# Performance work log

Measured on AMD Instinct MI355X. Metric: run time of the kernel, lower is better.

Reference implementation:

```python
import jax, jax.numpy as jnp
import numpy as np

NUM_CLASSES = 21
THRESH = 0.5
NEG_POS = 3
VAR0, VAR1 = 0.1, 0.2


def point_form(boxes):
    # center form (cx,cy,w,h) -> corner form (x1,y1,x2,y2)
    return jnp.concatenate([boxes[:, :2] - boxes[:, 2:] / 2,
                            boxes[:, :2] + boxes[:, 2:] / 2], axis=1)


def jaccard(a, b):
    # a: [N,4] corner form, b: [P,4] corner form -> IoU [N,P]
    lt = jnp.maximum(a[:, None, :2], b[None, :, :2])
    rb = jnp.minimum(a[:, None, 2:], b[None, :, 2:])
    wh = jnp.clip(rb - lt, 0.0)
    inter = wh[..., 0] * wh[..., 1]
    area_a = (a[:, 2] - a[:, 0]) * (a[:, 3] - a[:, 1])
    area_b = (b[:, 2] - b[:, 0]) * (b[:, 3] - b[:, 1])
    return inter / (area_a[:, None] + area_b[None, :] - inter)


def match_one(truths, labels, priors):
    # truths: [N,4] corner form, labels: [N] int, priors: [P,4] center form
    ov = jaccard(truths, point_form(priors))            # [N,P]
    best_prior_idx = jnp.argmax(ov, axis=1)             # [N] best prior per truth
    best_truth_ov = jnp.max(ov, axis=0)                 # [P]
    best_truth_idx = jnp.argmax(ov, axis=0)             # [P]
    # ensure each truth keeps its best prior
    best_truth_ov = best_truth_ov.at[best_prior_idx].set(2.0)
    best_truth_idx = best_truth_idx.at[best_prior_idx].set(
        jnp.arange(truths.shape[0], dtype=best_truth_idx.dtype))
    matches = truths[best_truth_idx]                    # [P,4]
    conf = labels[best_truth_idx] + 1                   # [P]
    conf = jnp.where(best_truth_ov < THRESH, 0, conf)
    # encode
    g_cxcy = ((matches[:, :2] + matches[:, 2:]) / 2 - priors[:, :2]) / (VAR0 * priors[:, 2:])
    g_wh = jnp.log((matches[:, 2:] - matches[:, :2]) / priors[:, 2:]) / VAR1
    return jnp.concatenate([g_cxcy, g_wh], axis=1), conf


def setup_inputs() -> dict:
    key = jax.random.key(0)
    k1, k2, k3, k4, k5, k6, k7 = jax.random.split(key, 7)
    B, P, C, N = 64, 24564, NUM_CLASSES, 16
    loc_data = jax.random.normal(k1, (B, P, 4), dtype=jnp.float32)
    conf_data = jax.random.normal(k2, (B, P, C), dtype=jnp.float32)
    # priors: valid center-form boxes
    ctr = 0.05 + 0.9 * jax.random.uniform(k3, (P, 2), dtype=jnp.float32)
    pwh = 0.05 + 0.25 * jax.random.uniform(k4, (P, 2), dtype=jnp.float32)
    priors = jnp.concatenate([ctr, pwh], axis=1)
    # truths: valid corner-form boxes
    xy1 = 0.7 * jax.random.uniform(k5, (B, N, 2), dtype=jnp.float32)
    twh = 0.05 + 0.2 * jax.random.uniform(k6, (B, N, 2), dtype=jnp.float32)
    truths = jnp.concatenate([xy1, xy1 + twh], axis=2)
    labels = jax.random.randint(k7, (B, N), 0, 20, dtype=jnp.int32)
    return {"loc_data": loc_data, "conf_data": conf_data, "priors": priors,
            "truths": truths, "labels": labels}


def reference(loc_data, conf_data, priors, truths, labels):
    B, P, C = conf_data.shape
    loc_t, conf_t = jax.vmap(lambda t, l: match_one(t, l, priors))(truths, labels)
    pos = conf_t > 0                                     # [B,P]

    # localization smooth-L1, summed over positives
    diff = loc_data - loc_t
    ad = jnp.abs(diff)
    sl1 = jnp.where(ad < 1.0, 0.5 * diff * diff, ad - 0.5)
    loss_l = jnp.sum(sl1 * pos[..., None].astype(loc_data.dtype))

    # per-prior CE = logsumexp - logit at matched class
    lse = jax.nn.logsumexp(conf_data, axis=2)            # [B,P]
    gathered = jnp.take_along_axis(conf_data, conf_t[..., None].astype(jnp.int32), axis=2)[..., 0]
    loss_c_all = lse - gathered

    # hard-negative mining via double argsort rank (pos zeroed first)
    loss_c_mine = jnp.where(pos, 0.0, loss_c_all)
    idx_rank = jnp.argsort(jnp.argsort(-loss_c_mine, axis=1), axis=1)
    num_pos = jnp.sum(pos, axis=1, keepdims=True)        # [B,1]
    num_neg = jnp.minimum(NEG_POS * num_pos, P - 1)
    neg = idx_rank < num_neg

    mask = pos | neg
    loss_c = jnp.sum(jnp.where(mask, loss_c_all, 0.0))

    n = jnp.sum(num_pos).astype(loc_data.dtype)
    return loss_l / n, loss_c / n
```

## Files before the change

kernel.cpp:

```cpp
#include <hip/hip_runtime.h>
#include <cstdint>
#include <cstddef>

#define B_ 64
#define P_ 24564
#define C_ 21
#define N_ 16
#define NPL_ 96
#define THRESH_ 0.5f


__device__ inline void async_copy16(const float* g, float* l) {
    __builtin_amdgcn_global_load_lds(
        (const __attribute__((address_space(1))) void*)g,
        (__attribute__((address_space(3))) void*)l, 16, 0, 0);
}

__device__ inline float sl1_encode(float4 ld, float4 pr,
                                   float tx1, float ty1, float tx2, float ty2) {
    float gcx = ((tx1 + tx2) * 0.5f - pr.x) / (0.1f * pr.z);
    float gcy = ((ty1 + ty2) * 0.5f - pr.y) / (0.1f * pr.w);
    float gw  = __logf((tx2 - tx1) / pr.z) / 0.2f;
    float gh  = __logf((ty2 - ty1) / pr.w) / 0.2f;
    float g[4] = {gcx, gcy, gw, gh};
    float l[4] = {ld.x, ld.y, ld.z, ld.w};
    float s = 0.0f;
#pragma unroll
    for (int i = 0; i < 4; i++) {
        float d = l[i] - g[i];
        float ad = fabsf(d);
        s += (ad < 1.0f) ? 0.5f * d * d : ad - 0.5f;
    }
    return s;
}


__global__ __launch_bounds__(256, 6) void
kF_fused(const float* __restrict__ loc,
         const float* __restrict__ conf,
         const float* __restrict__ priors,
         const float* __restrict__ truths,
         const int* __restrict__ labels,
         float* __restrict__ mine,
         float* __restrict__ part_ll,
         float* __restrict__ part_pce,
         int* __restrict__ part_np,
         unsigned long long* __restrict__ part_key) {
    int b = blockIdx.y, bx = blockIdx.x, t = threadIdx.x;
    int wid = t >> 6, lane = t & 63;
    __shared__ float scf[256 * C_];
    __shared__ unsigned long long swk[N_ * 4];
    __shared__ int lb[N_];
    __shared__ float sll[4], spc[4];
    __shared__ int snp[4];

    int base_p = bx * 256;
    int nvalid = min(256, P_ - base_p);
    int maxf4 = (nvalid * C_) >> 2;
    const float* gtile = conf + ((size_t)b * P_ + base_p) * C_;

    for (int k = wid; k < 21; k += 4) {
        int f4 = k * 64 + lane;
        int s4 = (f4 < maxf4) ? f4 : (maxf4 - 1);
        async_copy16(gtile + (size_t)s4 * 4, scf + k * 256);
    }
    if (t < N_) lb[t] = labels[b * N_ + t];

    int p0 = base_p + t;
    bool valid = t < nvalid;
    float4 pr = ((const float4*)priors)[valid ? p0 : base_p];
    float px1 = pr.x - pr.z * 0.5f, py1 = pr.y - pr.w * 0.5f;
    float px2 = pr.x + pr.z * 0.5f, py2 = pr.y + pr.w * 0.5f;
    float ap = (px2 - px1) * (py2 - py1);

    float best = -1.0f;
    int bn = 0;
#pragma unroll
    for (int n = 0; n < N_; n++) {
        float4 tb = ((const float4*)truths)[b * N_ + n];
        float at = (tb.z - tb.x) * (tb.w - tb.y);
        float lx = fmaxf(tb.x, px1), ly = fmaxf(tb.y, py1);
        float rx = fminf(tb.z, px2), ry = fminf(tb.w, py2);
        float w = fmaxf(rx - lx, 0.0f), h = fmaxf(ry - ly, 0.0f);
        float inter = w * h;
        float iou = inter / (at + ap - inter);
        if (iou > best) { best = iou; bn = n; }

        unsigned k32 = valid ? __float_as_uint(iou) : 0u;
        unsigned m = k32;
#pragma unroll
        for (int off = 32; off; off >>= 1) {
            unsigned o = __shfl_xor(m, off);
            m = (o > m) ? o : m;
        }
        unsigned long long msk = __ballot(k32 == m);
        int wl = (int)__ffsll(msk) - 1;
        if (lane == 0)
            swk[n * 4 + wid] = ((unsigned long long)m << 32) |
                               (unsigned)~(unsigned)(base_p + (wid << 6) + wl);
    }
    int pos = (valid && best >= THRESH_) ? 1 : 0;

    __syncthreads();

    if (t < N_) {
        unsigned long long bk = swk[t * 4];
#pragma unroll
        for (int i = 1; i < 4; i++) {
            unsigned long long o = swk[t * 4 + i];
            bk = (o > bk) ? o : bk;
        }
        part_key[(size_t)(b * NPL_ + bx) * N_ + t] = bk;
    }

    float ll = 0.0f, pce = 0.0f;
    int np = 0;
    if (valid) {
        int cls = pos ? (lb[bn] + 1) : 0;
        float ssum = 0.0f;
#pragma unroll
        for (int i = 0; i < 21; i++) ssum += __expf(scf[t * 21 + i]);
        float g = scf[t * 21 + cls];
        float lca = fmaxf(__logf(ssum) - g, 0.0f);

        mine[(size_t)b * P_ + p0] = pos ? 0.0f : lca;

        if (pos) {
            np = 1;
            pce = lca;
            float4 ld = ((const float4*)loc)[(size_t)b * P_ + p0];
            float4 tb = ((const float4*)truths)[b * N_ + bn];
            ll = sl1_encode(ld, pr, tb.x, tb.y, tb.z, tb.w);
        }
    }

    for (int off = 32; off; off >>= 1) {
        ll += __shfl_down(ll, off);
        pce += __shfl_down(pce, off);
        np += __shfl_down(np, off);
    }
    if (lane == 0) { sll[wid] = ll; spc[wid] = pce; snp[wid] = np; }
    __syncthreads();
    if (t == 0) {
        float a = 0.0f, cc = 0.0f;
        int q = 0;
        for (int i = 0; i < 4; i++) { a += sll[i]; cc += spc[i]; q += snp[i]; }
        part_ll[b * NPL_ + bx] = a;
        part_pce[b * NPL_ + bx] = cc;
        part_np[b * NPL_ + bx] = q;
    }
}

__global__ __launch_bounds__(1024) void
kB_batch(const float* __restrict__ loc,
         const float* __restrict__ conf,
         const float* __restrict__ priors,
         const float* __restrict__ truths,
         const int* __restrict__ labels,
         const float* __restrict__ mine,
         const float* __restrict__ part_ll,
         const float* __restrict__ part_pce,
         const int* __restrict__ part_np,
         const unsigned long long* __restrict__ part_key,
         double* __restrict__ bll,
         double* __restrict__ bpc,
         int* __restrict__ bnp) {
    int b = blockIdx.x, t = threadIdx.x, wid = t >> 6, lane = t & 63;
    __shared__ float tr[N_ * 4];
    __shared__ int lb[N_];
    __shared__ unsigned long long skmax[N_];
    __shared__ int sp[N_];
    __shared__ float sdll, sdpce, sll_s, spc_s;
    __shared__ int sdnp, snp_s;
    __shared__ int scnt2[31];
    __shared__ float wsum[16];
    __shared__ int wcgt[16];

    if (t < N_ * 4) tr[t] = truths[b * N_ * 4 + t];
    if (t < N_) { lb[t] = labels[b * N_ + t]; skmax[t] = 0ull; }
    if (t < 31) scnt2[t] = 0;
    if (t == 0) { sdll = 0.f; sdpce = 0.f; sdnp = 0; sll_s = 0.f; spc_s = 0.f; snp_s = 0; }
    __syncthreads();
    if (t < 256) {
        int n = t & 15, j = t >> 4;
        unsigned long long bk = 0ull;
        for (int i = j; i < NPL_; i += 16) {
            unsigned long long k = part_key[(size_t)(b * NPL_ + i) * N_ + n];
            bk = (k > bk) ? k : bk;
        }
        atomicMax(&skmax[n], bk);
    }
    if (t < 128) {
        float a = 0.f, c2 = 0.f;
        int q = 0;
        if (t < NPL_) {
            a = part_ll[b * NPL_ + t];
            c2 = part_pce[b * NPL_ + t];
            q = part_np[b * NPL_ + t];
        }
        for (int off = 32; off; off >>= 1) {
            a += __shfl_down(a, off);
            c2 += __shfl_down(c2, off);
            q += __shfl_down(q, off);
        }
        if (lane == 0) {
            atomicAdd(&sll_s, a);
            atomicAdd(&spc_s, c2);
            atomicAdd(&snp_s, q);
        }
    }
    __syncthreads();
    if (t < N_) sp[t] = (int)~(unsigned)(skmax[t] & 0xFFFFFFFFull);
    __syncthreads();
    if (t < N_) {
        int p = sp[t];
        bool last = true;
        for (int n = t + 1; n < N_; n++) if (sp[n] == p) last = false;
        if (last) {
            int nf = t;
            float4 pr = ((const float4*)priors)[p];
            float px1 = pr.x - pr.z * 0.5f, py1 = pr.y - pr.w * 0.5f;
            float px2 = pr.x + pr.z * 0.5f, py2 = pr.y + pr.w * 0.5f;
            float ap = (px2 - px1) * (py2 - py1);
            float best = -1.0f;
            int bti = 0;
            for (int n = 0; n < N_; n++) {
                float tx1 = tr[n * 4], ty1 = tr[n * 4 + 1];
                float tx2 = tr[n * 4 + 2], ty2 = tr[n * 4 + 3];
                float at = (tx2 - tx1) * (ty2 - ty1);
                float lx = fmaxf(tx1, px1), ly = fmaxf(ty1, py1);
                float rx = fminf(tx2, px2), ry = fminf(ty2, py2);
                float w = fmaxf(rx - lx, 0.0f), h = fmaxf(ry - ly, 0.0f);
                float inter = w * h;
                float iou = inter / (at + ap - inter);
                if (iou > best) { best = iou; bti = n; }
            }
            int pos_old = (best >= THRESH_) ? 1 : 0;
            const float* cp = conf + ((size_t)b * P_ + p) * C_;
            float ssum = 0.0f;
            for (int j = 0; j < C_; j++) ssum += __expf(cp[j]);
            float lse = __logf(ssum);
            float4 ld = ((const float4*)loc)[(size_t)b * P_ + p];
            float dll = sl1_encode(ld, pr, tr[nf * 4], tr[nf * 4 + 1],
                                   tr[nf * 4 + 2], tr[nf * 4 + 3]);
            float dpce = lse - cp[lb[nf] + 1];
            int dnp = 1 - pos_old;
            if (pos_old) {
                dll -= sl1_encode(ld, pr, tr[bti * 4], tr[bti * 4 + 1],
                                  tr[bti * 4 + 2], tr[bti * 4 + 3]);
                dpce -= lse - cp[lb[bti] + 1];
            }
            atomicAdd(&sdll, dll);
            atomicAdd(&sdpce, dpce);
            atomicAdd(&sdnp, dnp);
        }
    }

    unsigned omask = 0;
#pragma unroll
    for (int n = 0; n < N_; n++) {
        int p = sp[n];
        if ((p & 1023) == t) omask |= 1u << (p >> 10);
    }
    const float* v = mine + (size_t)b * P_;
    int nel = (t < (P_ - 23 * 1024)) ? 24 : 23;
    float xv[24];
#pragma unroll
    for (int i = 0; i < 24; i++) {
        float x = 0.0f;
        if (i < nel) x = v[t + (i << 10)];
        if ((omask >> i) & 1) x = 0.0f;
        xv[i] = x;
    }
    __syncthreads();
    int np = snp_s + sdnp;
    int k = np * 3;
    if (k > P_ - 1) k = P_ - 1;

    unsigned T = 0u;
    for (int bpos = 30; bpos >= 0; bpos--) {
        unsigned cand = T | (1u << bpos);
        int c = 0;
#pragma unroll
        for (int i = 0; i < 24; i++)
            if (__float_as_uint(xv[i]) >= cand) c++;
        for (int off = 32; off; off >>= 1) c += __shfl_down(c, off);
        if (lane == 0) atomicAdd(&scnt2[30 - bpos], c);
        __syncthreads();
        int tot = scnt2[30 - bpos];
        T = (tot >= k) ? cand : T;
    }

    float psum = 0.0f;
    int cgt = 0;
#pragma unroll
    for (int i = 0; i < 24; i++) {
        if (__float_as_uint(xv[i]) > T) { psum += xv[i]; cgt++; }
    }
    for (int off = 32; off; off >>= 1) {
        psum += __shfl_down(psum, off);
        cgt += __shfl_down(cgt, off);
    }
    if (lane == 0) { wsum[wid] = psum; wcgt[wid] = cgt; }
    __syncthreads();
    if (t == 0) {
        float s2 = 0.0f;
        int cg = 0;
        for (int i = 0; i < 16; i++) { s2 += wsum[i]; cg += wcgt[i]; }
        int skrem = k - cg;
        double tot = (double)s2 + (double)skrem * (double)__uint_as_float(T);
        bll[b] = (double)(sll_s + sdll);
        bpc[b] = (double)(spc_s + sdpce) + tot;
        bnp[b] = np;
    }
}

__global__ void kC_final(const double* __restrict__ bll,
                         const double* __restrict__ bpc,
                         const int* __restrict__ bnp,
                         float* __restrict__ out) {
    int t = threadIdx.x;
    double a = bll[t], c = bpc[t];
    int n = bnp[t];
    for (int off = 32; off; off >>= 1) {
        a += __shfl_down(a, off);
        c += __shfl_down(c, off);
        n += __shfl_down(n, off);
    }
    if (t == 0) {
        double dn = (double)n;
        out[0] = (float)(a / dn);
        out[1] = (float)(c / dn);
    }
}


extern "C" void kernel_launch(void* const* d_in, const int* in_sizes, int n_in,
                              void* d_out, int out_size, void* d_ws, size_t ws_size,
                              hipStream_t stream) {
    const float* loc    = (const float*)d_in[0];
    const float* conf   = (const float*)d_in[1];
    const float* priors = (const float*)d_in[2];
    const float* truths = (const float*)d_in[3];
    const int*   labels = (const int*)d_in[4];
    float* out = (float*)d_out;

    char* ws = (char*)d_ws;
    unsigned long long* part_key = (unsigned long long*)(ws);
    float*  part_ll  = (float*)(ws + 786432);
    float*  part_pce = (float*)(ws + 811008);
    int*    part_np  = (int*)(ws + 835584);
    double* bll      = (double*)(ws + 860160);
    double* bpc      = (double*)(ws + 860672);
    int*    bnp      = (int*)(ws + 861184);
    float*  mine     = (float*)(ws + 1048576);

    hipLaunchKernelGGL(kF_fused, dim3(NPL_, B_), dim3(256), 0, stream,
                       loc, conf, priors, truths, labels,
                       mine, part_ll, part_pce, part_np, part_key);
    hipLaunchKernelGGL(kB_batch, dim3(B_), dim3(1024), 0, stream,
                       loc, conf, priors, truths, labels, mine,
                       part_ll, part_pce, part_np, part_key, bll, bpc, bnp);
    hipLaunchKernelGGL(kC_final, dim3(1), dim3(64), 0, stream, bll, bpc, bnp, out);
}
```

Before: 266.4 us.

## Split per-truth best-prior argmax into a separate kernel

Moves the per-truth argmax over priors out of the fused main kernel into a new small kernel. It runs 8x64 blocks, each handling two truths across all priors, and writes the best prior index directly. This removes sixteen wave reductions and ballots per thread block from the heavy conf-processing kernel, and removes the part_key partial writes and their reduction in the batch kernel. The cost is an extra kernel launch that recomputes IoU for every truth-prior pair serially over priors, with only 512 blocks of parallelism.

```diff
diff --git a/kernel.cpp b/kernel.cpp
--- a/kernel.cpp
+++ b/kernel.cpp
@@ -7,6 +7,7 @@
 #define C_ 21
 #define N_ 16
 #define NPL_ 96
+#define NTT_ 2
 #define THRESH_ 0.5f
 
 
@@ -35,6 +36,76 @@
 }
 
 
+__global__ __launch_bounds__(256) void
+kT_argmax(const float* __restrict__ priors,
+          const float* __restrict__ truths,
+          int* __restrict__ sp_g) {
+    int b = blockIdx.y, n0 = blockIdx.x * NTT_, t = threadIdx.x;
+    int wid = t >> 6, lane = t & 63;
+    __shared__ unsigned skk[NTT_ * 4];
+    __shared__ int skp[NTT_ * 4];
+
+    float4 tb0 = ((const float4*)truths)[b * N_ + n0];
+    float4 tb1 = ((const float4*)truths)[b * N_ + n0 + 1];
+    float at0 = (tb0.z - tb0.x) * (tb0.w - tb0.y);
+    float at1 = (tb1.z - tb1.x) * (tb1.w - tb1.y);
+
+    unsigned bk0 = 0u, bk1 = 0u;
+    int bp0 = 0, bp1 = 0;
+    for (int p = t; p < P_; p += 256) {
+        float4 pr = ((const float4*)priors)[p];
+        float px1 = pr.x - pr.z * 0.5f, py1 = pr.y - pr.w * 0.5f;
+        float px2 = pr.x + pr.z * 0.5f, py2 = pr.y + pr.w * 0.5f;
+        float ap = (px2 - px1) * (py2 - py1);
+        {
+            float lx = fmaxf(tb0.x, px1), ly = fmaxf(tb0.y, py1);
+            float rx = fminf(tb0.z, px2), ry = fminf(tb0.w, py2);
+            float w = fmaxf(rx - lx, 0.0f), h = fmaxf(ry - ly, 0.0f);
+            float inter = w * h;
+            float iou = inter / (at0 + ap - inter);
+            unsigned k = __float_as_uint(iou);
+            if (k > bk0) { bk0 = k; bp0 = p; }
+        }
+        {
+            float lx = fmaxf(tb1.x, px1), ly = fmaxf(tb1.y, py1);
+            float rx = fminf(tb1.z, px2), ry = fminf(tb1.w, py2);
+            float w = fmaxf(rx - lx, 0.0f), h = fmaxf(ry - ly, 0.0f);
+            float inter = w * h;
+            float iou = inter / (at1 + ap - inter);
+            unsigned k = __float_as_uint(iou);
+            if (k > bk1) { bk1 = k; bp1 = p; }
+        }
+    }
+    unsigned m0 = bk0, m1 = bk1;
+#pragma unroll
+    for (int off = 32; off; off >>= 1) {
+        unsigned o0 = __shfl_xor(m0, off); m0 = (o0 > m0) ? o0 : m0;
+        unsigned o1 = __shfl_xor(m1, off); m1 = (o1 > m1) ? o1 : m1;
+    }
+    int q0 = (bk0 == m0) ? bp0 : 0x7FFFFFFF;
+    int q1 = (bk1 == m1) ? bp1 : 0x7FFFFFFF;
+#pragma unroll
+    for (int off = 32; off; off >>= 1) {
+        int o0 = __shfl_xor(q0, off); q0 = (o0 < q0) ? o0 : q0;
+        int o1 = __shfl_xor(q1, off); q1 = (o1 < q1) ? o1 : q1;
+    }
+    if (lane == 0) {
+        skk[0 * 4 + wid] = m0; skp[0 * 4 + wid] = q0;
+        skk[1 * 4 + wid] = m1; skp[1 * 4 + wid] = q1;
+    }
+    __syncthreads();
+    if (t < NTT_) {
+        unsigned bm = skk[t * 4];
+        int bq = skp[t * 4];
+        for (int i = 1; i < 4; i++) {
+            unsigned m2 = skk[t * 4 + i];
+            int q2 = skp[t * 4 + i];
+            if (m2 > bm || (m2 == bm && q2 < bq)) { bm = m2; bq = q2; }
+        }
+        sp_g[b * N_ + n0 + t] = bq;
+    }
+}
+
 __global__ __launch_bounds__(256, 6) void
 kF_fused(const float* __restrict__ loc,
          const float* __restrict__ conf,
@@ -44,12 +115,10 @@
          float* __restrict__ mine,
          float* __restrict__ part_ll,
          float* __restrict__ part_pce,
-         int* __restrict__ part_np,
-         unsigned long long* __restrict__ part_key) {
+         int* __restrict__ part_np) {
     int b = blockIdx.y, bx = blockIdx.x, t = threadIdx.x;
     int wid = t >> 6, lane = t & 63;
     __shared__ float scf[256 * C_];
-    __shared__ unsigned long long swk[N_ * 4];
     __shared__ int lb[N_];
     __shared__ float sll[4], spc[4];
     __shared__ int snp[4];
@@ -85,33 +154,10 @@
         float inter = w * h;
         float iou = inter / (at + ap - inter);
         if (iou > best) { best = iou; bn = n; }
-
-        unsigned k32 = valid ? __float_as_uint(iou) : 0u;
-        unsigned m = k32;
-#pragma unroll
-        for (int off = 32; off; off >>= 1) {
-            unsigned o = __shfl_xor(m, off);
-            m = (o > m) ? o : m;
-        }
-        unsigned long long msk = __ballot(k32 == m);
-        int wl = (int)__ffsll(msk) - 1;
-        if (lane == 0)
-            swk[n * 4 + wid] = ((unsigned long long)m << 32) |
-                               (unsigned)~(unsigned)(base_p + (wid << 6) + wl);
     }
     int pos = (valid && best >= THRESH_) ? 1 : 0;
 
     __syncthreads();
-
-    if (t < N_) {
-        unsigned long long bk = swk[t * 4];
-#pragma unroll
-        for (int i = 1; i < 4; i++) {
-            unsigned long long o = swk[t * 4 + i];
-            bk = (o > bk) ? o : bk;
-        }
-        part_key[(size_t)(b * NPL_ + bx) * N_ + t] = bk;
-    }
 
     float ll = 0.0f, pce = 0.0f;
     int np = 0;
@@ -161,14 +207,13 @@
          const float* __restrict__ part_ll,
          const float* __restrict__ part_pce,
          const int* __restrict__ part_np,
-         const unsigned long long* __restrict__ part_key,
+         const int* __restrict__ sp_g,
          double* __restrict__ bll,
          double* __restrict__ bpc,
          int* __restrict__ bnp) {
     int b = blockIdx.x, t = threadIdx.x, wid = t >> 6, lane = t & 63;
     __shared__ float tr[N_ * 4];
     __shared__ int lb[N_];
-    __shared__ unsigned long long skmax[N_];
     __shared__ int sp[N_];
     __shared__ float sdll, sdpce, sll_s, spc_s;
     __shared__ int sdnp, snp_s;
@@ -177,19 +222,15 @@
     __shared__ int wcgt[16];
 
     if (t < N_ * 4) tr[t] = truths[b * N_ * 4 + t];
-    if (t < N_) { lb[t] = labels[b * N_ + t]; skmax[t] = 0ull; }
+    if (t < N_) {
+        lb[t] = labels[b * N_ + t];
+        int pv = sp_g[b * N_ + t];
+        sp[t] = (pv < 0) ? 0 : ((pv >= P_) ? (P_ - 1) : pv);
+    }
     if (t < 31) scnt2[t] = 0;
     if (t == 0) { sdll = 0.f; sdpce = 0.f; sdnp = 0; sll_s = 0.f; spc_s = 0.f; snp_s = 0; }
     __syncthreads();
-    if (t < 256) {
-        int n = t & 15, j = t >> 4;
-        unsigned long long bk = 0ull;
-        for (int i = j; i < NPL_; i += 16) {
-            unsigned long long k = part_key[(size_t)(b * NPL_ + i) * N_ + n];
-            bk = (k > bk) ? k : bk;
-        }
-        atomicMax(&skmax[n], bk);
-    }
+
     if (t < 128) {
         float a = 0.f, c2 = 0.f;
         int q = 0;
@@ -209,9 +250,6 @@
             atomicAdd(&snp_s, q);
         }
     }
-    __syncthreads();
-    if (t < N_) sp[t] = (int)~(unsigned)(skmax[t] & 0xFFFFFFFFull);
-    __syncthreads();
     if (t < N_) {
         int p = sp[t];
         bool last = true;
@@ -346,7 +384,7 @@
     float* out = (float*)d_out;
 
     char* ws = (char*)d_ws;
-    unsigned long long* part_key = (unsigned long long*)(ws);
+    int*    sp_g     = (int*)(ws);
     float*  part_ll  = (float*)(ws + 786432);
     float*  part_pce = (float*)(ws + 811008);
     int*    part_np  = (int*)(ws + 835584);
@@ -355,11 +393,13 @@
     int*    bnp      = (int*)(ws + 861184);
     float*  mine     = (float*)(ws + 1048576);
 
+    hipLaunchKernelGGL(kT_argmax, dim3(N_ / NTT_, B_), dim3(256), 0, stream,
+                       priors, truths, sp_g);
     hipLaunchKernelGGL(kF_fused, dim3(NPL_, B_), dim3(256), 0, stream,
                        loc, conf, priors, truths, labels,
-                       mine, part_ll, part_pce, part_np, part_key);
+                       mine, part_ll, part_pce, part_np);
     hipLaunchKernelGGL(kB_batch, dim3(B_), dim3(1024), 0, stream,
                        loc, conf, priors, truths, labels, mine,
-                       part_ll, part_pce, part_np, part_key, bll, bpc, bnp);
+                       part_ll, part_pce, part_np, sp_g, bll, bpc, bnp);
     hipLaunchKernelGGL(kC_final, dim3(1), dim3(64), 0, stream, bll, bpc, bnp, out);
 }
```

Result: slower. 353.5 us (+32.7%).

## Replace bitwise radix threshold search with 3-pass histogram select; per-wave conf staging

Applied to the files above, without the earlier changes.

The hard-negative top-k threshold search used 31 sequential bit passes, each with a block-wide count and a barrier. It is replaced by a three-level radix histogram select (11/10/10 bits) over LDS with replicated sub-histograms and a wave-level prefix scan. In the fused kernel, each wave now loads only its own slice of the conf tile and waits with s_waitcnt, so the first block barrier can be dropped. Labels are read directly instead of through shared memory. The new select uses more LDS and relies on atomics, which may contend on skewed float distributions.

```diff
diff --git a/kernel.cpp b/kernel.cpp
--- a/kernel.cpp
+++ b/kernel.cpp
@@ -32,6 +32,30 @@
         s += (ad < 1.0f) ? 0.5f * d * d : ad - 0.5f;
     }
     return s;
+}
+
+__device__ inline void scan_hist(const int* h, int M, int kk,
+                                 int* outB, int* outR) {
+    int lane = threadIdx.x & 63;
+    int CH = M >> 6;
+    int base = M - (lane + 1) * CH;
+    int s = 0;
+    for (int j = 0; j < CH; j++) s += h[base + j];
+    int incl = s;
+#pragma unroll
+    for (int off = 1; off < 64; off <<= 1) {
+        int v = __shfl_up(incl, off);
+        if (lane >= off) incl += v;
+    }
+    int excl = incl - s;
+    if (excl < kk && excl + s >= kk) {
+        int acc = excl;
+        for (int bin = base + CH - 1; bin >= base; bin--) {
+            int c = h[bin];
+            if (acc + c >= kk) { *outB = bin; *outR = kk - acc; break; }
+            acc += c;
+        }
+    }
 }
 
 
@@ -48,9 +72,8 @@
          unsigned long long* __restrict__ part_key) {
     int b = blockIdx.y, bx = blockIdx.x, t = threadIdx.x;
     int wid = t >> 6, lane = t & 63;
-    __shared__ float scf[256 * C_];
+    __shared__ float scf[4 * 1536];
     __shared__ unsigned long long swk[N_ * 4];
-    __shared__ int lb[N_];
     __shared__ float sll[4], spc[4];
     __shared__ int snp[4];
 
@@ -58,13 +81,6 @@
     int nvalid = min(256, P_ - base_p);
     int maxf4 = (nvalid * C_) >> 2;
     const float* gtile = conf + ((size_t)b * P_ + base_p) * C_;
-
-    for (int k = wid; k < 21; k += 4) {
-        int f4 = k * 64 + lane;
-        int s4 = (f4 < maxf4) ? f4 : (maxf4 - 1);
-        async_copy16(gtile + (size_t)s4 * 4, scf + k * 256);
-    }
-    if (t < N_) lb[t] = labels[b * N_ + t];
 
     int p0 = base_p + t;
     bool valid = t < nvalid;
@@ -73,18 +89,28 @@
     float px2 = pr.x + pr.z * 0.5f, py2 = pr.y + pr.w * 0.5f;
     float ap = (px2 - px1) * (py2 - py1);
 
+    float* slice = scf + wid * 1536;
+    int wf4 = wid * 336;
+#pragma unroll
+    for (int i = 0; i < 6; i++) {
+        int f4 = wf4 + i * 64 + lane;
+        int s4 = (f4 < maxf4) ? f4 : (maxf4 - 1);
+        async_copy16(gtile + (size_t)s4 * 4, slice + i * 256);
+    }
+
     float best = -1.0f;
-    int bn = 0;
+    int bn = 0, bl = 0;
 #pragma unroll
     for (int n = 0; n < N_; n++) {
         float4 tb = ((const float4*)truths)[b * N_ + n];
+        int ln = labels[b * N_ + n];
         float at = (tb.z - tb.x) * (tb.w - tb.y);
         float lx = fmaxf(tb.x, px1), ly = fmaxf(tb.y, py1);
         float rx = fminf(tb.z, px2), ry = fminf(tb.w, py2);
         float w = fmaxf(rx - lx, 0.0f), h = fmaxf(ry - ly, 0.0f);
         float inter = w * h;
         float iou = inter / (at + ap - inter);
-        if (iou > best) { best = iou; bn = n; }
+        if (iou > best) { best = iou; bn = n; bl = ln; }
 
         unsigned k32 = valid ? __float_as_uint(iou) : 0u;
         unsigned m = k32;
@@ -101,26 +127,17 @@
     }
     int pos = (valid && best >= THRESH_) ? 1 : 0;
 
-    __syncthreads();
-
-    if (t < N_) {
-        unsigned long long bk = swk[t * 4];
-#pragma unroll
-        for (int i = 1; i < 4; i++) {
-            unsigned long long o = swk[t * 4 + i];
-            bk = (o > bk) ? o : bk;
-        }
-        part_key[(size_t)(b * NPL_ + bx) * N_ + t] = bk;
-    }
+    asm volatile("s_waitcnt vmcnt(0)" ::: "memory");
 
     float ll = 0.0f, pce = 0.0f;
     int np = 0;
     if (valid) {
-        int cls = pos ? (lb[bn] + 1) : 0;
+        int cls = pos ? (bl + 1) : 0;
+        const float* row = scf + wid * 1536 + lane * 21;
         float ssum = 0.0f;
 #pragma unroll
-        for (int i = 0; i < 21; i++) ssum += __expf(scf[t * 21 + i]);
-        float g = scf[t * 21 + cls];
+        for (int i = 0; i < 21; i++) ssum += __expf(row[i]);
+        float g = row[cls];
         float lca = fmaxf(__logf(ssum) - g, 0.0f);
 
         mine[(size_t)b * P_ + p0] = pos ? 0.0f : lca;
@@ -140,7 +157,17 @@
         np += __shfl_down(np, off);
     }
     if (lane == 0) { sll[wid] = ll; spc[wid] = pce; snp[wid] = np; }
-    __syncthreads();
+
+    __syncthreads();
+    if (t < N_) {
+        unsigned long long bk = swk[t * 4];
+#pragma unroll
+        for (int i = 1; i < 4; i++) {
+            unsigned long long o = swk[t * 4 + i];
+            bk = (o > bk) ? o : bk;
+        }
+        part_key[(size_t)(b * NPL_ + bx) * N_ + t] = bk;
+    }
     if (t == 0) {
         float a = 0.0f, cc = 0.0f;
         int q = 0;
@@ -172,13 +199,19 @@
     __shared__ int sp[N_];
     __shared__ float sdll, sdpce, sll_s, spc_s;
     __shared__ int sdnp, snp_s;
-    __shared__ int scnt2[31];
+    __shared__ int hist[4 * 2048];
+    __shared__ int hist2[1024];
+    __shared__ int hist3[1024];
+    __shared__ int sB[3], sR[3];
     __shared__ float wsum[16];
     __shared__ int wcgt[16];
 
     if (t < N_ * 4) tr[t] = truths[b * N_ * 4 + t];
     if (t < N_) { lb[t] = labels[b * N_ + t]; skmax[t] = 0ull; }
-    if (t < 31) scnt2[t] = 0;
+#pragma unroll
+    for (int i = 0; i < 8; i++) hist[t + (i << 10)] = 0;
+    hist2[t] = 0;
+    hist3[t] = 0;
     if (t == 0) { sdll = 0.f; sdpce = 0.f; sdnp = 0; sll_s = 0.f; spc_s = 0.f; snp_s = 0; }
     __syncthreads();
     if (t < 256) {
@@ -272,23 +305,57 @@
         if ((omask >> i) & 1) x = 0.0f;
         xv[i] = x;
     }
-    __syncthreads();
+
+    int rep = (wid & 3) << 11;
+#pragma unroll
+    for (int i = 0; i < 24; i++) {
+        if (i < nel) {
+            unsigned bb = __float_as_uint(xv[i]);
+            atomicAdd(&hist[rep + (bb >> 20)], 1);
+        }
+    }
+    __syncthreads();
+    {
+        int h0 = hist[t] + hist[t + 2048] + hist[t + 4096] + hist[t + 6144];
+        int h1 = hist[t + 1024] + hist[t + 3072] + hist[t + 5120] + hist[t + 7168];
+        hist[t] = h0;
+        hist[t + 1024] = h1;
+    }
+    __syncthreads();
+
     int np = snp_s + sdnp;
     int k = np * 3;
     if (k > P_ - 1) k = P_ - 1;
 
-    unsigned T = 0u;
-    for (int bpos = 30; bpos >= 0; bpos--) {
-        unsigned cand = T | (1u << bpos);
-        int c = 0;
-#pragma unroll
-        for (int i = 0; i < 24; i++)
-            if (__float_as_uint(xv[i]) >= cand) c++;
-        for (int off = 32; off; off >>= 1) c += __shfl_down(c, off);
-        if (lane == 0) atomicAdd(&scnt2[30 - bpos], c);
+    unsigned T = 0x7FFFFFFFu;
+    if (k > 0) {
+        if (wid == 0) scan_hist(hist, 2048, k, &sB[0], &sR[0]);
         __syncthreads();
-        int tot = scnt2[30 - bpos];
-        T = (tot >= k) ? cand : T;
+        unsigned B1 = (unsigned)sB[0];
+        int k1 = sR[0];
+#pragma unroll
+        for (int i = 0; i < 24; i++) {
+            if (i < nel) {
+                unsigned bb = __float_as_uint(xv[i]);
+                if ((bb >> 20) == B1) atomicAdd(&hist2[(bb >> 10) & 0x3FF], 1);
+            }
+        }
+        __syncthreads();
+        if (wid == 0) scan_hist(hist2, 1024, k1, &sB[1], &sR[1]);
+        __syncthreads();
+        unsigned hi = (B1 << 10) | (unsigned)sB[1];
+        int k2 = sR[1];
+#pragma unroll
+        for (int i = 0; i < 24; i++) {
+            if (i < nel) {
+                unsigned bb = __float_as_uint(xv[i]);
+                if ((bb >> 10) == hi) atomicAdd(&hist3[bb & 0x3FF], 1);
+            }
+        }
+        __syncthreads();
+        if (wid == 0) scan_hist(hist3, 1024, k2, &sB[2], &sR[2]);
+        __syncthreads();
+        T = (hi << 10) | (unsigned)sB[2];
     }
 
     float psum = 0.0f;
```

Measured after the change: 232.6 us, median of 2. 1.15x faster.
